# Kernel tuning notes

Measured on AMD Instinct MI355X. Metric: run time of the kernel, lower is better.

The kernel has to match this reference:

```python
import jax, jax.numpy as jnp
import numpy as np

N = 8192      # nodes
D = 256       # feature dim
GAMMA = 10.0
EPS = 1e-6
DIAG_FILL = -1e-6
# std = 0 in DGM.__init__ default -> the normal(mean=0, std=0) noise is exactly zero, so it is omitted.


def _embed(x, W, edges):
    # minimal message-passing embed_f: h = relu(xW + sum_{(s,d) in E} (xW)[s] -> d)
    h = x @ W
    agg = jax.ops.segment_sum(h[edges[0]], edges[1], num_segments=N)
    return jax.nn.relu(h + agg)


def _cdist(x):
    # pairwise euclidean distance, [N, N]
    sq = jnp.sum(x * x, axis=-1)
    d2 = sq[:, None] + sq[None, :] - 2.0 * (x @ x.T)
    return jnp.sqrt(jnp.clip(d2, 0.0))


def _layernorm(z, gamma, beta):
    # scalar-affine LayerNorm with unbiased std (torch x.std default ddof=1)
    mean = jnp.mean(z, axis=-1, keepdims=True)
    std = jnp.std(z, axis=-1, ddof=1, keepdims=True)
    return gamma * (z - mean) / (std + EPS) + beta


def _entmax15(z):
    # 1.5-entmax over last axis (Peters et al. 2019, exact sort-based algorithm)
    z = z / 2.0
    z = z - jnp.max(z, axis=-1, keepdims=True)
    zs = -jnp.sort(-z, axis=-1)                      # descending sort per row
    k = jnp.arange(1, z.shape[-1] + 1, dtype=z.dtype)
    mean = jnp.cumsum(zs, axis=-1) / k
    meansq = jnp.cumsum(zs * zs, axis=-1) / k
    ss = k * (meansq - mean * mean)
    delta = (1.0 - ss) / k
    tau = mean - jnp.sqrt(jnp.clip(delta, 0.0))
    support = jnp.sum(tau <= zs, axis=-1)            # support size per row
    tau_star = jnp.take_along_axis(tau, (support - 1)[..., None], axis=-1)
    p = jnp.clip(z - tau_star, 0.0)
    return p * p


def setup_inputs() -> dict:
    key = jax.random.key(0)
    k1, k2, k3 = jax.random.split(key, 3)
    x = jax.random.normal(k1, (N, D), dtype=jnp.float32)
    edges = jax.random.randint(k2, (2, 262144), 0, N)
    W = jax.random.normal(k3, (D, D), dtype=jnp.float32) * (1.0 / np.sqrt(D))
    gamma = jnp.full((1,), GAMMA, dtype=jnp.float32)
    beta = jnp.zeros((1,), dtype=jnp.float32)
    return {"x": x, "W": W, "gamma": gamma, "beta": beta, "edges": edges}


def reference(x, W, gamma, beta, edges):
    h = _embed(x, W, edges)                          # [N, D]
    probs = -_cdist(h)                               # [N, N]
    zn = _layernorm(probs, gamma, beta)
    idx = jnp.arange(N)
    zn = zn.at[idx, idx].set(DIAG_FILL)              # fill_diagonal_(-1e-6)
    vprobs = _entmax15(zn)                           # [N, N]
    res = (((vprobs + vprobs.T) * 0.5) > 0).astype(jnp.int32)
    logprobs = jnp.sum(res, axis=1)
    # NOTE: torch returns res.nonzero().t_() (data-dependent shape); we return the
    # equivalent dense adjacency `res` to stay jit-compatible.
    return h, res, logprobs
```

## Files before the change

### kernel.cpp

```cpp
#include <hip/hip_runtime.h>

#define N_NODES 8192
#define NMASK 8191
#define DIMF 256
#define LN_EPS 1e-6f
#define DIAG_Z (-5e-7f)
#define QSCALE 256.0f
#define QINV (1.0f / 256.0f)
#define BK 16
#define LDA 40

typedef float f32x4 __attribute__((ext_vector_type(4)));
typedef unsigned short ushort8v __attribute__((ext_vector_type(8)));
typedef short short8v __attribute__((ext_vector_type(8)));

__device__ __forceinline__ unsigned short f2bf(float f) {
  unsigned int u = __float_as_uint(f);
  u = (u + 0x7FFFu + ((u >> 16) & 1u)) >> 16;
  return (unsigned short)u;
}
__device__ __forceinline__ float bf2f(unsigned short s) {
  return __uint_as_float(((unsigned int)s) << 16);
}

__global__ void DGM_22857815949798_kernel() {}

__global__ __launch_bounds__(256) void DGM_22857815949798_dtp(const unsigned short* __restrict__ W16,
                                                              int hint, int* __restrict__ flag) {
  __shared__ float red[4];
  const int t = threadIdx.x;
  if (hint == 0 || hint == 1) { if (t == 0) flag[0] = hint; return; }
  float m = 0.f;
  for (int i = t; i < 2048; i += 256) {
    float v = fabsf(bf2f(W16[i]));
    if (!(v < 1e6f)) v = 1e6f;
    m += v;
  }
#pragma unroll
  for (int o = 32; o; o >>= 1) m += __shfl_down(m, o);
  if ((t & 63) == 0) red[t >> 6] = m;
  __syncthreads();
  if (t == 0) flag[0] = ((red[0] + red[1] + red[2] + red[3]) * (1.0f / 2048.0f) < 10.0f) ? 1 : 0;
}

__global__ __launch_bounds__(256) void DGM_22857815949798_init(int* deg, int* cursor) {
  int i = blockIdx.x * 256 + threadIdx.x;
  if (i < N_NODES) { deg[i] = 0; cursor[i] = 0; }
}

__global__ __launch_bounds__(256) void DGM_22857815949798_e1(const void* __restrict__ xv,
                                                             const void* __restrict__ Wv,
                                                             const int* __restrict__ flag,
                                                             float* __restrict__ h0) {
  __shared__ float xs[4][DIMF];
  const int bf = *flag;
  const int t = threadIdx.x;
  const int r0 = blockIdx.x * 4;
#pragma unroll
  for (int r = 0; r < 4; ++r) {
    size_t idx = (size_t)(r0 + r) * DIMF + t;
    xs[r][t] = bf ? bf2f(((const unsigned short*)xv)[idx]) : ((const float*)xv)[idx];
  }
  __syncthreads();
  float a0 = 0.f, a1 = 0.f, a2 = 0.f, a3 = 0.f;
  for (int k = 0; k < DIMF; ++k) {
    size_t wi = (size_t)k * DIMF + t;
    float w = bf ? bf2f(((const unsigned short*)Wv)[wi]) : ((const float*)Wv)[wi];
    a0 = fmaf(xs[0][k], w, a0);
    a1 = fmaf(xs[1][k], w, a1);
    a2 = fmaf(xs[2][k], w, a2);
    a3 = fmaf(xs[3][k], w, a3);
  }
  h0[(size_t)(r0 + 0) * DIMF + t] = a0;
  h0[(size_t)(r0 + 1) * DIMF + t] = a1;
  h0[(size_t)(r0 + 2) * DIMF + t] = a2;
  h0[(size_t)(r0 + 3) * DIMF + t] = a3;
}

__global__ __launch_bounds__(256) void DGM_22857815949798_deg(const int* __restrict__ dst,
                                                              int* __restrict__ deg, int E) {
  int e = blockIdx.x * 256 + threadIdx.x;
  if (e < E) atomicAdd(&deg[dst[e] & NMASK], 1);
}

__global__ __launch_bounds__(256) void DGM_22857815949798_scan(const int* __restrict__ deg,
                                                               int* __restrict__ off) {
  __shared__ int part[256];
  const int t = threadIdx.x;
  const int base = t * 32;
  int loc[32];
  int s = 0;
#pragma unroll
  for (int q = 0; q < 32; ++q) { loc[q] = s; s += deg[base + q]; }
  part[t] = s;
  __syncthreads();
  for (int o = 1; o < 256; o <<= 1) {
    int v = (t >= o) ? part[t - o] : 0;
    __syncthreads();
    part[t] += v;
    __syncthreads();
  }
  int excl = (t == 0) ? 0 : part[t - 1];
#pragma unroll
  for (int q = 0; q < 32; ++q) off[base + q] = excl + loc[q];
  if (t == 255) off[N_NODES] = excl + s;
}

__global__ __launch_bounds__(256) void DGM_22857815949798_scatter(const int* __restrict__ src,
                                                                  const int* __restrict__ dst,
                                                                  const int* __restrict__ off,
                                                                  int* __restrict__ cursor,
                                                                  int* __restrict__ adj, int E) {
  int e = blockIdx.x * 256 + threadIdx.x;
  if (e < E) {
    int d = dst[e] & NMASK;
    int p = atomicAdd(&cursor[d], 1);
    unsigned w = (unsigned)(off[d] + p);
    if (w < (unsigned)E) adj[w] = src[e] & NMASK;
  }
}

__global__ __launch_bounds__(256) void DGM_22857815949798_embed(const float* __restrict__ h0,
                                                                const int* __restrict__ adj,
                                                                const int* __restrict__ off,
                                                                void* __restrict__ hout, int outf,
                                                                float* __restrict__ sq) {
  __shared__ float rbuf[4];
  const int d = blockIdx.x;
  const int c = threadIdx.x;
  const int lane = c & 63, wv = c >> 6;
  int beg = off[d], end = off[d + 1];
  if (beg < 0) beg = 0;
  if (end > 262144) end = 262144;
  float v = h0[(size_t)d * DIMF + c];
  for (int e = beg; e < end; ++e) {
    int s = adj[e] & NMASK;
    v += h0[(size_t)s * DIMF + c];
  }
  v = fmaxf(v, 0.f);
  size_t idx = (size_t)d * DIMF + c;
  float vb;
  if (outf) { ((float*)hout)[idx] = v; vb = v; }
  else { unsigned short us = f2bf(v); ((unsigned short*)hout)[idx] = us; vb = bf2f(us); }
  float p = vb * vb;
#pragma unroll
  for (int o = 32; o; o >>= 1) p += __shfl_down(p, o);
  if (lane == 0) rbuf[wv] = p;
  __syncthreads();
  if (c == 0) sq[d] = rbuf[0] + rbuf[1] + rbuf[2] + rbuf[3];
}

__global__ __launch_bounds__(256) void DGM_22857815949798_gramm(const unsigned short* __restrict__ H,
                                                                const float* __restrict__ sq,
                                                                unsigned short* __restrict__ dq) {
  __shared__ __align__(16) unsigned short lds[16384];
  unsigned short* Alds = lds;
  unsigned short* Blds = lds + 128 * LDA;
  const int t = threadIdx.x;
  const int lane = t & 63, wv = t >> 6;
  const int i0 = blockIdx.y * 128, j0 = blockIdx.x * 128;
  const int wM = (wv >> 1) * 64, wN = (wv & 1) * 64;
  const int quad = lane >> 4, cid = lane & 15;
  const int arow = t >> 2;
  const int kcol = (t & 3) * 8;

  const unsigned short* gA = H + (size_t)(i0 + arow) * DIMF + kcol;
  const unsigned short* gB = H + (size_t)(j0 + arow) * DIMF + kcol;

  f32x4 acc[4][4] = {};

  for (int ko = 0; ko < 8; ++ko) {
    const int kk = ko * 32;
    ushort8v a0 = *(const ushort8v*)(gA + kk);
    ushort8v a1 = *(const ushort8v*)(gA + (size_t)64 * DIMF + kk);
    ushort8v b0 = *(const ushort8v*)(gB + kk);
    ushort8v b1 = *(const ushort8v*)(gB + (size_t)64 * DIMF + kk);
    __syncthreads();
    *(ushort8v*)(Alds + arow * LDA + kcol) = a0;
    *(ushort8v*)(Alds + (arow + 64) * LDA + kcol) = a1;
    *(ushort8v*)(Blds + arow * LDA + kcol) = b0;
    *(ushort8v*)(Blds + (arow + 64) * LDA + kcol) = b1;
    __syncthreads();

    short8v af[4], bq[4];
#pragma unroll
    for (int mi = 0; mi < 4; ++mi)
      af[mi] = *(const short8v*)(Alds + (wM + mi * 16 + cid) * LDA + quad * 8);
#pragma unroll
    for (int ni = 0; ni < 4; ++ni)
      bq[ni] = *(const short8v*)(Blds + (wN + ni * 16 + cid) * LDA + quad * 8);
#pragma unroll
    for (int mi = 0; mi < 4; ++mi)
#pragma unroll
      for (int ni = 0; ni < 4; ++ni)
        acc[mi][ni] = __builtin_amdgcn_mfma_f32_16x16x32_bf16(af[mi], bq[ni], acc[mi][ni], 0, 0, 0);
  }
  __syncthreads();

  unsigned short* wbuf = lds + wv * 4096;
#pragma unroll
  for (int mi = 0; mi < 4; ++mi) {
#pragma unroll
    for (int r = 0; r < 4; ++r) {
      const int lrow = mi * 16 + quad * 4 + r;
      const int gi = i0 + wM + lrow;
      const float si = sq[gi];
#pragma unroll
      for (int ni = 0; ni < 4; ++ni) {
        const int gj = j0 + wN + ni * 16 + cid;
        float d2 = si + sq[gj] - 2.0f * acc[mi][ni][r];
        float dd = (gi == gj) ? 0.0f : sqrtf(fmaxf(d2, 0.0f));
        int u = (int)(dd * QSCALE + 0.5f);
        u = (u > 65535) ? 65535 : u;
        wbuf[lrow * 64 + ni * 16 + cid] = (unsigned short)u;
      }
    }
  }
#pragma unroll
  for (int it = 0; it < 8; ++it) {
    int o = it * 512 + lane * 8;
    int row = o >> 6;
    int col = o & 63;
    size_t goff = (size_t)(i0 + wM + row) * N_NODES + (size_t)(j0 + wN + col);
    *(ushort8v*)(dq + goff) = *(const ushort8v*)(wbuf + o);
  }
}

__global__ __launch_bounds__(256) void DGM_22857815949798_gram(const void* __restrict__ Hv,
                                                               const float* __restrict__ sq,
                                                               void* __restrict__ Dv, int outf) {
  __shared__ float Al[BK][128];
  __shared__ float Bl[BK][128];
  __shared__ float sqi[128], sqj[128];
  const int t = threadIdx.x;

  const int bt = blockIdx.x;
  int bi = (int)((129.0f - sqrtf(129.0f * 129.0f - 8.0f * (float)bt)) * 0.5f);
  if (bi < 0) bi = 0;
  if (bi > 63) bi = 63;
  while (bi * (129 - bi) / 2 > bt) --bi;
  while ((bi + 1) * (128 - bi) / 2 <= bt) ++bi;
  const int bj = bi + (bt - bi * (129 - bi) / 2);
  const int i0 = bi * 128, j0 = bj * 128;

  const int srow = t >> 1;
  const int skh = (t & 1) * 8;
  const size_t aoff = (size_t)(i0 + srow) * DIMF + skh;
  const size_t boff = (size_t)(j0 + srow) * DIMF + skh;

  if (t < 128) sqi[t] = sq[i0 + t];
  else sqj[t - 128] = sq[j0 + t - 128];

  const int tx = t & 15, ty = t >> 4;
  float acc[8][8] = {};

  for (int ko = 0; ko < DIMF / BK; ++ko) {
    float a8[8], b8[8];
    if (outf) {
      const float* gA = (const float*)Hv + aoff + ko * BK;
      const float* gB = (const float*)Hv + boff + ko * BK;
      f32x4 x0 = *(const f32x4*)gA, x1 = *(const f32x4*)(gA + 4);
      f32x4 y0 = *(const f32x4*)gB, y1 = *(const f32x4*)(gB + 4);
#pragma unroll
      for (int q = 0; q < 4; ++q) { a8[q] = x0[q]; a8[q + 4] = x1[q]; b8[q] = y0[q]; b8[q + 4] = y1[q]; }
    } else {
      ushort8v av = *(const ushort8v*)((const unsigned short*)Hv + aoff + ko * BK);
      ushort8v bv = *(const ushort8v*)((const unsigned short*)Hv + boff + ko * BK);
#pragma unroll
      for (int q = 0; q < 8; ++q) { a8[q] = bf2f(av[q]); b8[q] = bf2f(bv[q]); }
    }
    __syncthreads();
#pragma unroll
    for (int q = 0; q < 8; ++q) {
      Al[skh + q][srow] = a8[q];
      Bl[skh + q][srow] = b8[q];
    }
    __syncthreads();
#pragma unroll
    for (int kk = 0; kk < BK; ++kk) {
      f32x4 a0 = *(const f32x4*)(&Al[kk][ty * 8]);
      f32x4 a1 = *(const f32x4*)(&Al[kk][ty * 8 + 4]);
      f32x4 b0 = *(const f32x4*)(&Bl[kk][tx * 8]);
      f32x4 b1 = *(const f32x4*)(&Bl[kk][tx * 8 + 4]);
#pragma unroll
      for (int r = 0; r < 8; ++r) {
        float ar = (r < 4) ? a0[r] : a1[r - 4];
#pragma unroll
        for (int c = 0; c < 4; ++c) {
          acc[r][c] = fmaf(ar, b0[c], acc[r][c]);
          acc[r][c + 4] = fmaf(ar, b1[c], acc[r][c + 4]);
        }
      }
    }
  }

#pragma unroll
  for (int r = 0; r < 8; ++r) {
    const int gi = i0 + ty * 8 + r;
    const float si = sqi[ty * 8 + r];
    float ddv[8];
#pragma unroll
    for (int c = 0; c < 8; ++c) {
      const int gj = j0 + tx * 8 + c;
      float d2 = si + sqj[tx * 8 + c] - 2.0f * acc[r][c];
      ddv[c] = (gi == gj) ? 0.0f : sqrtf(fmaxf(d2, 0.0f));
    }
    size_t go = (size_t)gi * N_NODES + (j0 + tx * 8);
    if (outf) {
      f32x4 o0, o1;
#pragma unroll
      for (int c = 0; c < 4; ++c) { o0[c] = ddv[c]; o1[c] = ddv[c + 4]; }
      *(f32x4*)((float*)Dv + go) = o0;
      *(f32x4*)((float*)Dv + go + 4) = o1;
    } else {
      ushort8v ov;
#pragma unroll
      for (int c = 0; c < 8; ++c) {
        int u = (int)(ddv[c] * QSCALE + 0.5f);
        ov[c] = (unsigned short)((u > 65535) ? 65535 : u);
      }
      *(ushort8v*)((unsigned short*)Dv + go) = ov;
    }
  }
  if (bi != bj) {
#pragma unroll
    for (int c = 0; c < 8; ++c) {
      const int gj = j0 + tx * 8 + c;
      const float sj = sqj[tx * 8 + c];
      float ddv[8];
#pragma unroll
      for (int r = 0; r < 8; ++r) {
        float d2 = sqi[ty * 8 + r] + sj - 2.0f * acc[r][c];
        ddv[r] = sqrtf(fmaxf(d2, 0.0f));
      }
      size_t go = (size_t)gj * N_NODES + (i0 + ty * 8);
      if (outf) {
        f32x4 o0, o1;
#pragma unroll
        for (int r = 0; r < 4; ++r) { o0[r] = ddv[r]; o1[r] = ddv[r + 4]; }
        *(f32x4*)((float*)Dv + go) = o0;
        *(f32x4*)((float*)Dv + go + 4) = o1;
      } else {
        ushort8v ov;
#pragma unroll
        for (int r = 0; r < 8; ++r) {
          int u = (int)(ddv[r] * QSCALE + 0.5f);
          ov[r] = (unsigned short)((u > 65535) ? 65535 : u);
        }
        *(ushort8v*)((unsigned short*)Dv + go) = ov;
      }
    }
  }
}

__global__ __launch_bounds__(256) void DGM_22857815949798_tau(const void* __restrict__ Dv, int outf,
                                                              const void* __restrict__ gv,
                                                              const void* __restrict__ bv,
                                                              const int* __restrict__ flag,
                                                              float* __restrict__ dthr,
                                                              float* __restrict__ taug) {
  __shared__ float cand[N_NODES];
  __shared__ int ccount;
  __shared__ float redS[4], redM[4];
  __shared__ float bc[4];
  const int i = blockIdx.x;
  const int t = threadIdx.x;
  const int lane = t & 63, wv = t >> 6;

  float dv[32];
  float sum = 0.f, dmin = 1e30f;
#pragma unroll
  for (int q = 0; q < 4; ++q) {
    const int j0 = q * 2048 + t * 8;
    const size_t go = (size_t)i * N_NODES + j0;
    if (outf) {
      f32x4 p0 = *(const f32x4*)((const float*)Dv + go);
      f32x4 p1 = *(const f32x4*)((const float*)Dv + go + 4);
#pragma unroll
      for (int e = 0; e < 8; ++e) dv[q * 8 + e] = (e < 4) ? p0[e] : p1[e - 4];
    } else {
      ushort8v pk = *(const ushort8v*)((const unsigned short*)Dv + go);
#pragma unroll
      for (int e = 0; e < 8; ++e) dv[q * 8 + e] = (float)pk[e] * QINV;
    }
#pragma unroll
    for (int e = 0; e < 8; ++e) {
      float d = dv[q * 8 + e];
      sum += d;
      if (j0 + e != i) dmin = fminf(dmin, d);
    }
  }
#pragma unroll
  for (int o = 32; o; o >>= 1) {
    sum += __shfl_down(sum, o);
    dmin = fminf(dmin, __shfl_down(dmin, o));
  }
  if (lane == 0) { redS[wv] = sum; redM[wv] = dmin; }
  __syncthreads();
  if (t == 0) {
    float S = redS[0] + redS[1] + redS[2] + redS[3];
    bc[0] = S * (1.0f / (float)N_NODES);
    bc[1] = fminf(fminf(redM[0], redM[1]), fminf(redM[2], redM[3]));
  }
  __syncthreads();
  const float mean = bc[0];
  float ss = 0.f;
#pragma unroll
  for (int q = 0; q < 32; ++q) { float u = dv[q] - mean; ss += u * u; }
#pragma unroll
  for (int o = 32; o; o >>= 1) ss += __shfl_down(ss, o);
  if (lane == 0) redS[wv] = ss;
  __syncthreads();
  if (t == 0) {
    float Q = redS[0] + redS[1] + redS[2] + redS[3];
    float sd = sqrtf(fmaxf(Q * (1.0f / (float)(N_NODES - 1)), 0.f));
    int bf = *flag;
    float gamma = bf ? bf2f(((const unsigned short*)gv)[0]) : ((const float*)gv)[0];
    float beta = bf ? bf2f(((const unsigned short*)bv)[0]) : ((const float*)bv)[0];
    float a = gamma / (2.0f * (sd + LN_EPS));
    float hb = 0.5f * beta;
    float zmax = fmaxf(a * (mean - bc[1]) + hb, DIAG_Z);
    bc[1] = a; bc[2] = zmax; bc[3] = hb;
    ccount = 0;
  }
  __syncthreads();
  const float a = bc[1], zmax = bc[2], hb = bc[3];
  const float zlo = zmax - 1.0f;
#pragma unroll
  for (int q = 0; q < 4; ++q) {
#pragma unroll
    for (int e = 0; e < 8; ++e) {
      const int j = q * 2048 + t * 8 + e;
      float z = a * (mean - dv[q * 8 + e]) + hb;
      if (j == i) z = DIAG_Z;
      if (z > zlo) {
        int p = atomicAdd(&ccount, 1);
        if (p < N_NODES) cand[p] = z;
      }
    }
  }
  __syncthreads();
  if (wv == 0) {
    const int n = (ccount < N_NODES) ? ccount : N_NODES;
    float lo = zlo, hi = zmax;
    for (int it = 0; it < 30; ++it) {
      float mid = 0.5f * (lo + hi);
      float s = 0.f;
      for (int p = lane; p < n; p += 64) {
        float u = cand[p] - mid;
        s += (u > 0.f) ? u * u : 0.f;
      }
#pragma unroll
      for (int o = 32; o; o >>= 1) s += __shfl_down(s, o);
      s = __shfl(s, 0);
      if (s > 1.f) lo = mid; else hi = mid;
    }
    if (lane == 0) {
      float tau = 0.5f * (lo + hi);
      taug[i] = tau;
      dthr[i] = mean - (tau - hb) / a;
    }
  }
}

__global__ __launch_bounds__(256) void DGM_22857815949798_res(void* __restrict__ Dv, int outf,
                                                              const float* __restrict__ dthr,
                                                              const float* __restrict__ taug,
                                                              void* __restrict__ lp) {
  __shared__ int redc[4];
  const int i = blockIdx.x;
  const int t = threadIdx.x;
  const int lane = t & 63, wv = t >> 6;
  const float di = dthr[i];
  const float ti = taug[i];
  int c = 0;
#pragma unroll
  for (int q = 0; q < 4; ++q) {
    const int j0 = q * 2048 + t * 8;
    const size_t go = (size_t)i * N_NODES + j0;
    float dvv[8];
    if (outf) {
      f32x4 p0 = *(const f32x4*)((const float*)Dv + go);
      f32x4 p1 = *(const f32x4*)((const float*)Dv + go + 4);
#pragma unroll
      for (int e = 0; e < 8; ++e) dvv[e] = (e < 4) ? p0[e] : p1[e - 4];
    } else {
      ushort8v pk = *(const ushort8v*)((const unsigned short*)Dv + go);
#pragma unroll
      for (int e = 0; e < 8; ++e) dvv[e] = (float)pk[e] * QINV;
    }
    f32x4 c0 = *(const f32x4*)(dthr + j0);
    f32x4 c1 = *(const f32x4*)(dthr + j0 + 4);
    bool rr[8];
#pragma unroll
    for (int e = 0; e < 8; ++e) {
      float dj = (e < 4) ? c0[e] : c1[e - 4];
      bool r = (dvv[e] < di) || (dvv[e] < dj);
      if (j0 + e == i) r = (DIAG_Z > ti);
      rr[e] = r;
      c += r ? 1 : 0;
    }
    if (outf) {
      f32x4 o0, o1;
#pragma unroll
      for (int e = 0; e < 4; ++e) { o0[e] = rr[e] ? 1.0f : 0.0f; o1[e] = rr[e + 4] ? 1.0f : 0.0f; }
      *(f32x4*)((float*)Dv + go) = o0;
      *(f32x4*)((float*)Dv + go + 4) = o1;
    } else {
      ushort8v ob;
#pragma unroll
      for (int e = 0; e < 8; ++e) ob[e] = rr[e] ? (unsigned short)0x3F80 : (unsigned short)0;
      *(ushort8v*)((unsigned short*)Dv + go) = ob;
    }
  }
#pragma unroll
  for (int o = 32; o; o >>= 1) c += __shfl_down(c, o);
  if (lane == 0) redc[wv] = c;
  __syncthreads();
  if (t == 0) {
    int tot = redc[0] + redc[1] + redc[2] + redc[3];
    if (outf) ((float*)lp)[i] = (float)tot;
    else ((unsigned short*)lp)[i] = f2bf((float)tot);
  }
}

static bool DGM_rng(const void* p, void** start, size_t* sz) {
  void* st = nullptr;
  size_t s = 0;
  if (hipPointerGetAttribute(&st, HIP_POINTER_ATTRIBUTE_RANGE_START_ADDR,
                             (hipDeviceptr_t)p) != hipSuccess) return false;
  if (hipPointerGetAttribute(&s, HIP_POINTER_ATTRIBUTE_RANGE_SIZE,
                             (hipDeviceptr_t)p) != hipSuccess) return false;
  *start = st; *sz = s;
  return true;
}
static bool DGM_exactish(size_t s, size_t x) { return s >= x && s < x + (size_t)(2u << 20); }

extern "C" int kernel_launch(void* const* d_in, const int* in_sizes, int n_in,
                             void* d_out, int out_size, void* d_ws, size_t ws_size,
                             hipStream_t stream) {
  (void)n_in; (void)out_size; (void)ws_size;

  int curdev = 0;
  (void)hipGetDevice(&curdev);
  int tgtdev = curdev;
  hipPointerAttribute_t pa;
  if (hipPointerGetAttributes(&pa, d_out) == hipSuccess) {
    if (pa.device >= 0 && pa.device < 64) tgtdev = pa.device;
  }
  if (tgtdev != curdev) (void)hipSetDevice(tgtdev);

  hipStreamCaptureStatus cap = hipStreamCaptureStatusNone;
  hipError_t se = hipStreamIsCapturing(stream, &cap);
  const bool validStream = (se == hipSuccess);
  const bool capturing = validStream && (cap != hipStreamCaptureStatusNone);
  hipStream_t s = validStream ? stream : (hipStream_t)0;

  const size_t OUT_B16 = 134238208ull;
  const size_t OUT_B32 = 268476416ull;
  void* outp = d_out;
  void* wsp = d_ws;
  int outf = 0;
  {
    void* st3 = nullptr; size_t s3 = 0; bool ok3 = DGM_rng(d_out, &st3, &s3);
    void* st5 = nullptr; size_t s5 = 0; bool ok5 = DGM_rng(d_ws, &st5, &s5);
    if (ok3 && st3 == d_out && DGM_exactish(s3, OUT_B16)) { outp = d_out; wsp = d_ws; outf = 0; }
    else if (ok3 && st3 == d_out && DGM_exactish(s3, OUT_B32)) { outp = d_out; wsp = d_ws; outf = 1; }
    else if (ok5 && st5 == d_ws && DGM_exactish(s5, OUT_B16)) { outp = d_ws; wsp = d_out; outf = 0; }
    else if (ok5 && st5 == d_ws && DGM_exactish(s5, OUT_B32)) { outp = d_ws; wsp = d_out; outf = 1; }
    else if (ok3 && s3 >= (200u << 20)) { outf = 1; }
  }

  int hint = -1;
  {
    void* stx = nullptr; size_t sx = 0;
    if (DGM_rng(d_in[0], &stx, &sx) && stx == d_in[0]) {
      if (DGM_exactish(sx, 4194304ull)) hint = 1;
      else if (DGM_exactish(sx, 8388608ull)) hint = 0;
    }
  }

  int E = in_sizes[4] / 2;
  if (E <= 0 || E > 8388608) E = 262144;
  const int* edges = (const int*)d_in[4];
  const int* esrc = edges;
  const int* edst = edges + E;

  const size_t esz = outf ? 4 : 2;
  char* ob = (char*)outp;
  void* h_area = ob;
  void* res_area = ob + (size_t)N_NODES * DIMF * esz;
  void* lp_area = ob + ((size_t)N_NODES * DIMF + (size_t)N_NODES * N_NODES) * esz;

  char* R = (char*)res_area;
  float* h0 = (float*)R;
  int* adj = (int*)(R + 8u * 1024 * 1024);
  int* deg = (int*)(R + 9u * 1024 * 1024);
  int* cursor = (int*)(R + 9u * 1024 * 1024 + 32768);
  int* off = (int*)(R + 9u * 1024 * 1024 + 65536);

  int* flag = (int*)wsp;
  float* sq = (float*)((char*)wsp + 4096);
  float* dthr = (float*)((char*)wsp + 4096 + 32768);
  float* taug = (float*)((char*)wsp + 4096 + 65536);

  (void)hipGetLastError();

  DGM_22857815949798_dtp<<<1, 256, 0, s>>>((const unsigned short*)d_in[1], hint, flag);
  DGM_22857815949798_init<<<N_NODES / 256, 256, 0, s>>>(deg, cursor);
  DGM_22857815949798_e1<<<N_NODES / 4, 256, 0, s>>>(d_in[0], d_in[1], flag, h0);
  DGM_22857815949798_deg<<<(E + 255) / 256, 256, 0, s>>>(edst, deg, E);
  DGM_22857815949798_scan<<<1, 256, 0, s>>>(deg, off);
  DGM_22857815949798_scatter<<<(E + 255) / 256, 256, 0, s>>>(esrc, edst, off, cursor, adj, E);
  DGM_22857815949798_embed<<<N_NODES, 256, 0, s>>>(h0, adj, off, h_area, outf, sq);
  if (outf) {
    DGM_22857815949798_gram<<<2080, 256, 0, s>>>(h_area, sq, res_area, outf);
  } else {
    dim3 gg(N_NODES / 128, N_NODES / 128);
    DGM_22857815949798_gramm<<<gg, 256, 0, s>>>((const unsigned short*)h_area, sq,
                                                (unsigned short*)res_area);
  }
  DGM_22857815949798_tau<<<N_NODES, 256, 0, s>>>(res_area, outf, d_in[2], d_in[3], flag, dthr, taug);
  DGM_22857815949798_res<<<N_NODES, 256, 0, s>>>(res_area, outf, dthr, taug, lp_area);

  hipError_t err = hipGetLastError();
  if (!capturing) {
    if (err != hipSuccess) {
      (void)hipDeviceSynchronize();
      (void)hipGetLastError();
    }
    (void)hipStreamSynchronize(s);
  }

  if (tgtdev != curdev) (void)hipSetDevice(curdev);
  return 0;
}

extern "C" int launch(void* const* a, const int* b, int c, void* d, int e, void* f,
                      size_t g, hipStream_t h) { return kernel_launch(a, b, c, d, e, f, g, h); }
extern "C" int run(void* const* a, const int* b, int c, void* d, int e, void* f,
                   size_t g, hipStream_t h) { return kernel_launch(a, b, c, d, e, f, g, h); }
extern "C" int kernel_main(void* const* a, const int* b, int c, void* d, int e, void* f,
                           size_t g, hipStream_t h) { return kernel_launch(a, b, c, d, e, f, g, h); }
extern "C" int DGM_22857815949798(void* const* a, const int* b, int c, void* d, int e, void* f,
                                  size_t g, hipStream_t h) { return kernel_launch(a, b, c, d, e, f, g, h); }
```

Before: 764.5 us.

## Use split-bf16 MFMA for the fp32 Gram distance kernel

Replaces the scalar-FMA fp32 Gram kernel, used when the input is fp32, with an MFMA kernel. Each fp32 value is split into a bf16 high part and a bf16 low residual, and three bf16 MFMAs (hi*hi, hi*lo, lo*hi) approximate the fp32 product. The aim is to move the N x N x D Gram matrix onto the matrix cores while keeping the triangular tiling and the mirrored write. The trade-off is slightly lower precision than true fp32 and more LDS traffic. The row-major write now uses scalar stores, which may be less coalesced.

```diff
diff --git a/kernel.cpp b/kernel.cpp
--- a/kernel.cpp
+++ b/kernel.cpp
@@ -150,6 +150,123 @@
   if (c == 0) sq[d] = rbuf[0] + rbuf[1] + rbuf[2] + rbuf[3];
 }
 
+__global__ __launch_bounds__(256) void DGM_22857815949798_gramf(const float* __restrict__ H,
+                                                                const float* __restrict__ sq,
+                                                                float* __restrict__ dq) {
+  __shared__ __align__(16) unsigned short Ahi[128 * LDA];
+  __shared__ __align__(16) unsigned short Alo[128 * LDA];
+  __shared__ __align__(16) unsigned short Bhi[128 * LDA];
+  __shared__ __align__(16) unsigned short Blo[128 * LDA];
+  __shared__ float sqi[128], sqj[128];
+  const int t = threadIdx.x;
+  const int lane = t & 63, wv = t >> 6;
+  const int quad = lane >> 4, cid = lane & 15;
+
+  const int bt = blockIdx.x;
+  int bi = (int)((129.0f - sqrtf(129.0f * 129.0f - 8.0f * (float)bt)) * 0.5f);
+  if (bi < 0) bi = 0;
+  if (bi > 63) bi = 63;
+  while (bi * (129 - bi) / 2 > bt) --bi;
+  while ((bi + 1) * (128 - bi) / 2 <= bt) ++bi;
+  const int bj = bi + (bt - bi * (129 - bi) / 2);
+  const int i0 = bi * 128, j0 = bj * 128;
+
+  const int wM = (wv >> 1) * 64, wN = (wv & 1) * 64;
+  const int srow = t >> 1;
+  const int khalf = (t & 1) * 16;
+
+  if (t < 128) sqi[t] = sq[i0 + t];
+  else sqj[t - 128] = sq[j0 + t - 128];
+
+  const float* pa = H + (size_t)(i0 + srow) * DIMF + khalf;
+  const float* pb = H + (size_t)(j0 + srow) * DIMF + khalf;
+
+  f32x4 acc[4][4] = {};
+
+  for (int ko = 0; ko < 8; ++ko) {
+    const int kk = ko * 32;
+    f32x4 av[4], bv[4];
+#pragma unroll
+    for (int q = 0; q < 4; ++q) {
+      av[q] = *(const f32x4*)(pa + kk + q * 4);
+      bv[q] = *(const f32x4*)(pb + kk + q * 4);
+    }
+    ushort8v ah[2], al[2], bh[2], bl[2];
+#pragma unroll
+    for (int q = 0; q < 4; ++q) {
+#pragma unroll
+      for (int e = 0; e < 4; ++e) {
+        const int idx = q * 4 + e;
+        const int hi8 = idx >> 3, lo8 = idx & 7;
+        float va = av[q][e];
+        unsigned int ua = __float_as_uint(va);
+        ah[hi8][lo8] = (unsigned short)(ua >> 16);
+        al[hi8][lo8] = f2bf(va - __uint_as_float(ua & 0xFFFF0000u));
+        float vb = bv[q][e];
+        unsigned int ub = __float_as_uint(vb);
+        bh[hi8][lo8] = (unsigned short)(ub >> 16);
+        bl[hi8][lo8] = f2bf(vb - __uint_as_float(ub & 0xFFFF0000u));
+      }
+    }
+    __syncthreads();
+    {
+      const int so = srow * LDA + khalf;
+      *(ushort8v*)(Ahi + so) = ah[0];
+      *(ushort8v*)(Ahi + so + 8) = ah[1];
+      *(ushort8v*)(Alo + so) = al[0];
+      *(ushort8v*)(Alo + so + 8) = al[1];
+      *(ushort8v*)(Bhi + so) = bh[0];
+      *(ushort8v*)(Bhi + so + 8) = bh[1];
+      *(ushort8v*)(Blo + so) = bl[0];
+      *(ushort8v*)(Blo + so + 8) = bl[1];
+    }
+    __syncthreads();
+
+    short8v fah[4], fal[4], fbh[4], fbl[4];
+#pragma unroll
+    for (int mi = 0; mi < 4; ++mi) {
+      const int ro = (wM + mi * 16 + cid) * LDA + quad * 8;
+      fah[mi] = *(const short8v*)(Ahi + ro);
+      fal[mi] = *(const short8v*)(Alo + ro);
+    }
+#pragma unroll
+    for (int ni = 0; ni < 4; ++ni) {
+      const int ro = (wN + ni * 16 + cid) * LDA + quad * 8;
+      fbh[ni] = *(const short8v*)(Bhi + ro);
+      fbl[ni] = *(const short8v*)(Blo + ro);
+    }
+#pragma unroll
+    for (int mi = 0; mi < 4; ++mi)
+#pragma unroll
+      for (int ni = 0; ni < 4; ++ni) {
+        acc[mi][ni] = __builtin_amdgcn_mfma_f32_16x16x32_bf16(fah[mi], fbh[ni], acc[mi][ni], 0, 0, 0);
+        acc[mi][ni] = __builtin_amdgcn_mfma_f32_16x16x32_bf16(fah[mi], fbl[ni], acc[mi][ni], 0, 0, 0);
+        acc[mi][ni] = __builtin_amdgcn_mfma_f32_16x16x32_bf16(fal[mi], fbh[ni], acc[mi][ni], 0, 0, 0);
+      }
+  }
+
+#pragma unroll
+  for (int mi = 0; mi < 4; ++mi) {
+    const int rbase = wM + mi * 16 + quad * 4;
+#pragma unroll
+    for (int ni = 0; ni < 4; ++ni) {
+      const int gj = j0 + wN + ni * 16 + cid;
+      const float sj = sqj[wN + ni * 16 + cid];
+      f32x4 dd;
+#pragma unroll
+      for (int r = 0; r < 4; ++r) {
+        const int gi = i0 + rbase + r;
+        float d2 = sqi[rbase + r] + sj - 2.0f * acc[mi][ni][r];
+        float d = (gi == gj) ? 0.0f : sqrtf(fmaxf(d2, 0.0f));
+        dd[r] = d;
+        dq[(size_t)gi * N_NODES + gj] = d;
+      }
+      if (bi != bj)
+        *(f32x4*)(dq + (size_t)gj * N_NODES + (i0 + rbase)) = dd;
+    }
+  }
+}
+
 __global__ __launch_bounds__(256) void DGM_22857815949798_gramm(const unsigned short* __restrict__ H,
                                                                 const float* __restrict__ sq,
                                                                 unsigned short* __restrict__ dq) {
@@ -226,133 +343,6 @@
   }
 }
 
-__global__ __launch_bounds__(256) void DGM_22857815949798_gram(const void* __restrict__ Hv,
-                                                               const float* __restrict__ sq,
-                                                               void* __restrict__ Dv, int outf) {
-  __shared__ float Al[BK][128];
-  __shared__ float Bl[BK][128];
-  __shared__ float sqi[128], sqj[128];
-  const int t = threadIdx.x;
-
-  const int bt = blockIdx.x;
-  int bi = (int)((129.0f - sqrtf(129.0f * 129.0f - 8.0f * (float)bt)) * 0.5f);
-  if (bi < 0) bi = 0;
-  if (bi > 63) bi = 63;
-  while (bi * (129 - bi) / 2 > bt) --bi;
-  while ((bi + 1) * (128 - bi) / 2 <= bt) ++bi;
-  const int bj = bi + (bt - bi * (129 - bi) / 2);
-  const int i0 = bi * 128, j0 = bj * 128;
-
-  const int srow = t >> 1;
-  const int skh = (t & 1) * 8;
-  const size_t aoff = (size_t)(i0 + srow) * DIMF + skh;
-  const size_t boff = (size_t)(j0 + srow) * DIMF + skh;
-
-  if (t < 128) sqi[t] = sq[i0 + t];
-  else sqj[t - 128] = sq[j0 + t - 128];
-
-  const int tx = t & 15, ty = t >> 4;
-  float acc[8][8] = {};
-
-  for (int ko = 0; ko < DIMF / BK; ++ko) {
-    float a8[8], b8[8];
-    if (outf) {
-      const float* gA = (const float*)Hv + aoff + ko * BK;
-      const float* gB = (const float*)Hv + boff + ko * BK;
-      f32x4 x0 = *(const f32x4*)gA, x1 = *(const f32x4*)(gA + 4);
-      f32x4 y0 = *(const f32x4*)gB, y1 = *(const f32x4*)(gB + 4);
-#pragma unroll
-      for (int q = 0; q < 4; ++q) { a8[q] = x0[q]; a8[q + 4] = x1[q]; b8[q] = y0[q]; b8[q + 4] = y1[q]; }
-    } else {
-      ushort8v av = *(const ushort8v*)((const unsigned short*)Hv + aoff + ko * BK);
-      ushort8v bv = *(const ushort8v*)((const unsigned short*)Hv + boff + ko * BK);
-#pragma unroll
-      for (int q = 0; q < 8; ++q) { a8[q] = bf2f(av[q]); b8[q] = bf2f(bv[q]); }
-    }
-    __syncthreads();
-#pragma unroll
-    for (int q = 0; q < 8; ++q) {
-      Al[skh + q][srow] = a8[q];
-      Bl[skh + q][srow] = b8[q];
-    }
-    __syncthreads();
-#pragma unroll
-    for (int kk = 0; kk < BK; ++kk) {
-      f32x4 a0 = *(const f32x4*)(&Al[kk][ty * 8]);
-      f32x4 a1 = *(const f32x4*)(&Al[kk][ty * 8 + 4]);
-      f32x4 b0 = *(const f32x4*)(&Bl[kk][tx * 8]);
-      f32x4 b1 = *(const f32x4*)(&Bl[kk][tx * 8 + 4]);
-#pragma unroll
-      for (int r = 0; r < 8; ++r) {
-        float ar = (r < 4) ? a0[r] : a1[r - 4];
-#pragma unroll
-        for (int c = 0; c < 4; ++c) {
-          acc[r][c] = fmaf(ar, b0[c], acc[r][c]);
-          acc[r][c + 4] = fmaf(ar, b1[c], acc[r][c + 4]);
-        }
-      }
-    }
-  }
-
-#pragma unroll
-  for (int r = 0; r < 8; ++r) {
-    const int gi = i0 + ty * 8 + r;
-    const float si = sqi[ty * 8 + r];
-    float ddv[8];
-#pragma unroll
-    for (int c = 0; c < 8; ++c) {
-      const int gj = j0 + tx * 8 + c;
-      float d2 = si + sqj[tx * 8 + c] - 2.0f * acc[r][c];
-      ddv[c] = (gi == gj) ? 0.0f : sqrtf(fmaxf(d2, 0.0f));
-    }
-    size_t go = (size_t)gi * N_NODES + (j0 + tx * 8);
-    if (outf) {
-      f32x4 o0, o1;
-#pragma unroll
-      for (int c = 0; c < 4; ++c) { o0[c] = ddv[c]; o1[c] = ddv[c + 4]; }
-      *(f32x4*)((float*)Dv + go) = o0;
-      *(f32x4*)((float*)Dv + go + 4) = o1;
-    } else {
-      ushort8v ov;
-#pragma unroll
-      for (int c = 0; c < 8; ++c) {
-        int u = (int)(ddv[c] * QSCALE + 0.5f);
-        ov[c] = (unsigned short)((u > 65535) ? 65535 : u);
-      }
-      *(ushort8v*)((unsigned short*)Dv + go) = ov;
-    }
-  }
-  if (bi != bj) {
-#pragma unroll
-    for (int c = 0; c < 8; ++c) {
-      const int gj = j0 + tx * 8 + c;
-      const float sj = sqj[tx * 8 + c];
-      float ddv[8];
-#pragma unroll
-      for (int r = 0; r < 8; ++r) {
-        float d2 = sqi[ty * 8 + r] + sj - 2.0f * acc[r][c];
-        ddv[r] = sqrtf(fmaxf(d2, 0.0f));
-      }
-      size_t go = (size_t)gj * N_NODES + (i0 + ty * 8);
-      if (outf) {
-        f32x4 o0, o1;
-#pragma unroll
-        for (int r = 0; r < 4; ++r) { o0[r] = ddv[r]; o1[r] = ddv[r + 4]; }
-        *(f32x4*)((float*)Dv + go) = o0;
-        *(f32x4*)((float*)Dv + go + 4) = o1;
-      } else {
-        ushort8v ov;
-#pragma unroll
-        for (int r = 0; r < 8; ++r) {
-          int u = (int)(ddv[r] * QSCALE + 0.5f);
-          ov[r] = (unsigned short)((u > 65535) ? 65535 : u);
-        }
-        *(ushort8v*)((unsigned short*)Dv + go) = ov;
-      }
-    }
-  }
-}
-
 __global__ __launch_bounds__(256) void DGM_22857815949798_tau(const void* __restrict__ Dv, int outf,
                                                               const void* __restrict__ gv,
                                                               const void* __restrict__ bv,
@@ -614,7 +604,7 @@
   DGM_22857815949798_scatter<<<(E + 255) / 256, 256, 0, s>>>(esrc, edst, off, cursor, adj, E);
   DGM_22857815949798_embed<<<N_NODES, 256, 0, s>>>(h0, adj, off, h_area, outf, sq);
   if (outf) {
-    DGM_22857815949798_gram<<<2080, 256, 0, s>>>(h_area, sq, res_area, outf);
+    DGM_22857815949798_gramf<<<2080, 256, 0, s>>>((const float*)h_area, sq, (float*)res_area);
   } else {
     dim3 gg(N_NODES / 128, N_NODES / 128);
     DGM_22857815949798_gramm<<<gg, 256, 0, s>>>((const unsigned short*)h_area, sq,
```

Result: faster. 664.8 us (-13.0%).
